# Kernel tuning notes

Hardware: AMD Instinct MI355X
Metric: run time of the kernel (lower is better)

Reference implementation:

```python
import jax, jax.numpy as jnp
import numpy as np

N_LEVELS = 16
N_FEATS = 2
TABLE_SIZE = 1 << 19          # log2_hashmap_size = 19
BASE_RES = 32
PER_LEVEL_SCALE = 1.3819
RES = 512
CLAMP = 25.133
PRIME_Y = np.uint32(2654435761)
N_PTS = 1 << 19


def hashgrid_encode(table, uv):
    """Instant-NGP style multires hashgrid. table: [L, T, F], uv: [N, 2] in [0,1].
    Returns [N, L*F]."""
    L, T, F = table.shape
    levels = jnp.arange(L)
    res = jnp.floor(BASE_RES * (PER_LEVEL_SCALE ** levels.astype(jnp.float32))).astype(jnp.int32)  # [L]
    # 4 bilinear corner offsets
    offs = jnp.array([[0, 0], [1, 0], [0, 1], [1, 1]], dtype=jnp.int32)  # [4, 2]

    def level_fn(tab_l, res_l):
        pos = uv * res_l.astype(uv.dtype)                       # [N, 2]
        p0 = jnp.clip(jnp.floor(pos).astype(jnp.int32), 0, res_l - 1)
        frac = pos - p0.astype(uv.dtype)                        # [N, 2]
        corners = p0[:, None, :] + offs[None, :, :]             # [N, 4, 2]
        cx = corners[..., 0].astype(jnp.uint32)
        cy = corners[..., 1].astype(jnp.uint32)
        stride = (res_l + 1).astype(jnp.uint32)
        dense_idx = cx + cy * stride                            # dense grid index
        hash_idx = (cx ^ (cy * PRIME_Y)) & jnp.uint32(T - 1)    # spatial hash (T is pow2)
        use_dense = (res_l + 1).astype(jnp.int64) * (res_l + 1).astype(jnp.int64) <= T
        idx = jnp.where(use_dense, dense_idx, hash_idx).astype(jnp.int32)  # [N, 4]
        feats = tab_l[idx]                                      # [N, 4, F] gather
        wx, wy = frac[:, 0], frac[:, 1]
        w = jnp.stack([(1 - wx) * (1 - wy), wx * (1 - wy),
                       (1 - wx) * wy, wx * wy], axis=-1)        # [N, 4]
        return jnp.einsum('ncf,nc->nf', feats, w)               # [N, F]

    out = jax.vmap(level_fn)(table, res)                        # [L, N, F]
    return out.transpose(1, 0, 2).reshape(uv.shape[0], L * F)


def sin_layer(x, W, b):
    h = jnp.clip(x @ W.T + b, -CLAMP, CLAMP)
    return jnp.sin(h)


def setup_inputs() -> dict:
    key = jax.random.key(0)
    ks = jax.random.split(key, 8)
    y = jax.random.randint(ks[0], (N_PTS,), 0, RES, dtype=jnp.int32)
    x = jax.random.randint(ks[1], (N_PTS,), 0, RES, dtype=jnp.int32)
    cam_feat = jax.random.normal(ks[2], (32,), dtype=jnp.float32)
    # NGP tables initialized uniform in [-1e-4, 1e-4]
    table = jax.random.uniform(ks[3], (N_LEVELS, TABLE_SIZE, N_FEATS),
                               minval=-1e-4, maxval=1e-4, dtype=jnp.float32)
    def siren_w(k, outp, inp):
        return jax.random.uniform(k, (outp, inp), minval=-1.0 / inp, maxval=1.0 / inp,
                                  dtype=jnp.float32)
    W1 = siren_w(ks[4], 512, 64)
    W2 = siren_w(ks[5], 512, 512)
    W3 = siren_w(ks[6], 384, 512)
    return {"y": y, "x": x, "cam_feat": cam_feat, "table": table,
            "W1": W1, "b1": jnp.zeros((512,), jnp.float32),
            "W2": W2, "b2": jnp.zeros((512,), jnp.float32),
            "W3": W3, "b3": jnp.zeros((384,), jnp.float32)}


def reference(y, x, cam_feat, table, W1, b1, W2, b2, W3, b3):
    denom = jnp.float32(RES - 1)
    uv = jnp.stack([jnp.clip(x.astype(jnp.float32), 0, RES - 1) / denom,
                    jnp.clip(y.astype(jnp.float32), 0, RES - 1) / denom], axis=-1)  # [N, 2]
    codes = hashgrid_encode(table, uv)                          # [N, 32]
    cam = jnp.broadcast_to(cam_feat[None, :], (codes.shape[0], cam_feat.shape[0]))
    h = jnp.concatenate([codes, cam], axis=-1)                  # [N, 64]
    h = sin_layer(h, W1, b1)
    h = sin_layer(h, W2, b2)
    return sin_layer(h, W3, b3)                                 # [N, 384]
```

## Files before the change

### kernel.cpp

```cpp
#include <hip/hip_runtime.h>

typedef _Float16 half8 __attribute__((ext_vector_type(8)));
typedef _Float16 half4 __attribute__((ext_vector_type(4)));
typedef _Float16 half2v __attribute__((ext_vector_type(2)));
typedef float f32x4 __attribute__((ext_vector_type(4)));

#define TSIZE (1 << 19)
#define TMASK (TSIZE - 1)

__constant__ int c_res[16] = {32, 44, 61, 84, 116, 161, 222, 307,
                              425, 588, 812, 1123, 1551, 2144, 2963, 4095};

__global__ void hg_cvt_all(const float* __restrict__ W1, const float* __restrict__ W2,
                           const float* __restrict__ W3, _Float16* __restrict__ d) {
  int g = blockIdx.x * blockDim.x + threadIdx.x;
  int i = g * 4;
  const float* s;
  if (i < 32768) s = W1 + i;
  else if (i < 32768 + 262144) s = W2 + (i - 32768);
  else s = W3 + (i - 32768 - 262144);
  float4 v = *(const float4*)s;
  half4 h = {(_Float16)v.x, (_Float16)v.y, (_Float16)v.z, (_Float16)v.w};
  *(half4*)(d + i) = h;
}

__device__ __forceinline__ float sin_act_precise(float x) {
  if (__builtin_expect(fabsf(x) > 1.0f, 0))
    return sinf(fminf(fmaxf(x, -25.133f), 25.133f));
  float x2 = x * x;
  float p = 2.75573192e-6f;
  p = fmaf(p, x2, -1.98412698e-4f);
  p = fmaf(p, x2, 8.33333333e-3f);
  p = fmaf(p, x2, -1.66666667e-1f);
  return fmaf(p * x2, x, x);
}

__device__ __forceinline__ float sin_act_fast(float x) {
  return __sinf(fminf(fmaxf(x, -25.133f), 25.133f));
}

#define XROW 144
#define SBASE 9216
#define SROW 1040
#define LD_X(m, k) (*(const half8*)(&smem[(m) * XROW + (k) * 2]))
#define LD_S(m, k) (*(const half8*)(&smem[SBASE + (m) * SROW + (k) * 2]))
#define ST_S8(m, n, v) \
  do { *(half4*)(&smem[SBASE + (m) * SROW + (n) * 2]) = (v); } while (0)

#define MFMA16 __builtin_amdgcn_mfma_f32_16x16x32_f16

__global__ void __launch_bounds__(512, 4)
hg_fused(const int* __restrict__ ybuf, const int* __restrict__ xbuf,
         const float* __restrict__ cam, const float* __restrict__ table,
         const _Float16* __restrict__ W1h, const float* __restrict__ b1,
         const _Float16* __restrict__ W2h, const float* __restrict__ b2,
         const _Float16* __restrict__ W3h, const float* __restrict__ b3,
         float* __restrict__ out) {
  __shared__ __align__(16) unsigned char smem[75776];
  const int t = threadIdx.x;
  const int lane = t & 63;
  const int wid = t >> 6;
  const int l15 = lane & 15;
  const int lhi = lane >> 4;
  const int pbase = blockIdx.x << 6;
  const f32x4 vzero = {0.f, 0.f, 0.f, 0.f};

  {
    const int sub = t & 15;
    const int res = c_res[sub];
    const float rf = (float)res;
    const unsigned strd = (unsigned)(res + 1);
    const bool dense = (res <= 723);
    const float* tb = table + ((size_t)sub * TSIZE) * 2;
    const float2 cf = ((const float2*)cam)[sub];
    const half2v hc = {(_Float16)cf.x, (_Float16)cf.y};
#pragma unroll
    for (int hh = 0; hh < 2; ++hh) {
      const int m = (t >> 4) + hh * 32;
      const int p = pbase + m;
      const float u = (float)xbuf[p] / 511.0f;
      const float v = (float)ybuf[p] / 511.0f;
      const float px = u * rf, py = v * rf;
      int p0x = (int)floorf(px); p0x = p0x < 0 ? 0 : (p0x > res - 1 ? res - 1 : p0x);
      int p0y = (int)floorf(py); p0y = p0y < 0 ? 0 : (p0y > res - 1 ? res - 1 : p0y);
      const float fx = px - (float)p0x, fy = py - (float)p0y;
      const float w00 = (1.f - fx) * (1.f - fy), w10 = fx * (1.f - fy);
      const float w01 = (1.f - fx) * fy, w11 = fx * fy;
      float c0 = 0.f, c1 = 0.f;
#pragma unroll
      for (int c = 0; c < 4; ++c) {
        const unsigned cx = (unsigned)(p0x + (c & 1));
        const unsigned cy = (unsigned)(p0y + (c >> 1));
        const unsigned idx = dense ? (cx + cy * strd)
                                   : ((cx ^ (cy * 2654435761u)) & TMASK);
        const float2 f = *(const float2*)(tb + (size_t)idx * 2);
        const float w = (c == 0) ? w00 : (c == 1) ? w10 : (c == 2) ? w01 : w11;
        c0 = fmaf(w, f.x, c0);
        c1 = fmaf(w, f.y, c1);
      }
      half2v hf = {(_Float16)c0, (_Float16)c1};
      *(half2v*)(&smem[m * XROW + 4 * sub]) = hf;
      *(half2v*)(&smem[m * XROW + 64 + 4 * sub]) = hc;
    }
  }
  __syncthreads();

  {
    const int n0 = wid << 6;
    f32x4 acc[4][4];
#pragma unroll
    for (int i = 0; i < 4; ++i)
#pragma unroll
      for (int j = 0; j < 4; ++j) acc[i][j] = vzero;
#pragma unroll
    for (int ks = 0; ks < 2; ++ks) {
      const int kk = ks * 32 + lhi * 8;
      half8 bw[4];
#pragma unroll
      for (int nf = 0; nf < 4; ++nf)
        bw[nf] = *(const half8*)(W1h + (n0 + nf * 16 + l15) * 64 + kk);
      half8 ax[4];
#pragma unroll
      for (int mf = 0; mf < 4; ++mf) ax[mf] = LD_X(mf * 16 + l15, kk);
#pragma unroll
      for (int mf = 0; mf < 4; ++mf)
#pragma unroll
        for (int nf = 0; nf < 4; ++nf)
          acc[mf][nf] = MFMA16(bw[nf], ax[mf], acc[mf][nf], 0, 0, 0);
    }
#pragma unroll
    for (int nf = 0; nf < 4; ++nf) {
      const int nb = n0 + nf * 16 + lhi * 4;
      const f32x4 bb = *(const f32x4*)(b1 + nb);
#pragma unroll
      for (int mf = 0; mf < 4; ++mf) {
        half4 pk;
#pragma unroll
        for (int r = 0; r < 4; ++r)
          pk[r] = (_Float16)sin_act_fast(acc[mf][nf][r] + bb[r]);
        ST_S8(mf * 16 + l15, nb, pk);
      }
    }
  }
  __syncthreads();

  {
    const int n0 = wid << 6;
    f32x4 acc[4][4];
#pragma unroll
    for (int i = 0; i < 4; ++i)
#pragma unroll
      for (int j = 0; j < 4; ++j) acc[i][j] = vzero;
#pragma unroll 2
    for (int ks = 0; ks < 16; ++ks) {
      const int kk = ks * 32 + lhi * 8;
      half8 bw[4];
#pragma unroll
      for (int nf = 0; nf < 4; ++nf)
        bw[nf] = *(const half8*)(W2h + (n0 + nf * 16 + l15) * 512 + kk);
      half8 ax[4];
#pragma unroll
      for (int mf = 0; mf < 4; ++mf) ax[mf] = LD_S(mf * 16 + l15, kk);
#pragma unroll
      for (int mf = 0; mf < 4; ++mf)
#pragma unroll
        for (int nf = 0; nf < 4; ++nf)
          acc[mf][nf] = MFMA16(bw[nf], ax[mf], acc[mf][nf], 0, 0, 0);
    }
#pragma unroll
    for (int nf = 0; nf < 4; ++nf) {
      const f32x4 bb = *(const f32x4*)(b2 + (n0 + nf * 16 + lhi * 4));
#pragma unroll
      for (int mf = 0; mf < 4; ++mf)
#pragma unroll
        for (int r = 0; r < 4; ++r)
          acc[mf][nf][r] = sin_act_fast(acc[mf][nf][r] + bb[r]);
    }
    __syncthreads();
#pragma unroll
    for (int nf = 0; nf < 4; ++nf) {
      const int nb = n0 + nf * 16 + lhi * 4;
#pragma unroll
      for (int mf = 0; mf < 4; ++mf) {
        half4 pk = {(_Float16)acc[mf][nf][0], (_Float16)acc[mf][nf][1],
                    (_Float16)acc[mf][nf][2], (_Float16)acc[mf][nf][3]};
        ST_S8(mf * 16 + l15, nb, pk);
      }
    }
  }
  __syncthreads();

  {
    const int n0 = wid * 48;
    f32x4 acc[4][3];
#pragma unroll
    for (int i = 0; i < 4; ++i)
#pragma unroll
      for (int j = 0; j < 3; ++j) acc[i][j] = vzero;
#pragma unroll 2
    for (int ks = 0; ks < 16; ++ks) {
      const int kk = ks * 32 + lhi * 8;
      half8 bw[3];
#pragma unroll
      for (int nf = 0; nf < 3; ++nf)
        bw[nf] = *(const half8*)(W3h + (n0 + nf * 16 + l15) * 512 + kk);
      half8 ax[4];
#pragma unroll
      for (int mf = 0; mf < 4; ++mf) ax[mf] = LD_S(mf * 16 + l15, kk);
#pragma unroll
      for (int mf = 0; mf < 4; ++mf)
#pragma unroll
        for (int nf = 0; nf < 3; ++nf)
          acc[mf][nf] = MFMA16(bw[nf], ax[mf], acc[mf][nf], 0, 0, 0);
    }
#pragma unroll
    for (int nf = 0; nf < 3; ++nf) {
      const int nb = n0 + nf * 16 + lhi * 4;
      const f32x4 bb = *(const f32x4*)(b3 + nb);
#pragma unroll
      for (int mf = 0; mf < 4; ++mf) {
        float4 o;
        float* op = &o.x;
#pragma unroll
        for (int r = 0; r < 4; ++r)
          op[r] = sin_act_precise(acc[mf][nf][r] + bb[r]);
        *(float4*)(out + (size_t)(pbase + mf * 16 + l15) * 384 + nb) = o;
      }
    }
  }
}

extern "C" void kernel_launch(void* const* d_in, const int* in_sizes, int n_in,
                              void* d_out, int out_size, void* d_ws, size_t ws_size,
                              hipStream_t stream) {
  const int* y = (const int*)d_in[0];
  const int* x = (const int*)d_in[1];
  const float* cam = (const float*)d_in[2];
  const float* table = (const float*)d_in[3];
  const float* W1 = (const float*)d_in[4];
  const float* b1 = (const float*)d_in[5];
  const float* W2 = (const float*)d_in[6];
  const float* b2 = (const float*)d_in[7];
  const float* W3 = (const float*)d_in[8];
  const float* b3 = (const float*)d_in[9];
  float* out = (float*)d_out;

  _Float16* Wh = (_Float16*)d_ws;
  _Float16* W1h = Wh;
  _Float16* W2h = W1h + 512 * 64;
  _Float16* W3h = W2h + 512 * 512;

  hg_cvt_all<<<480, 256, 0, stream>>>(W1, W2, W3, Wh);

  const int nblocks = (1 << 19) / 64;
  hg_fused<<<nblocks, 512, 0, stream>>>(y, x, cam, table, W1h, b1, W2h, b2, W3h, b3, out);
}
```

Measured before the change: 1.145 ms.

## Make fused kernel persistent over 8 tiles with double-buffered activations

Each block now processes eight 64-point tiles instead of one. It issues the hash-grid gather for the next tile during the layer-2 GEMM and computes the next tile's layer 1 into a second shared buffer while layer 3 runs. This is meant to hide gather latency behind MFMA work and to amortize the block prologue. In exchange it doubles shared memory to about 139 KB, which drops occupancy to fewer blocks per CU, and leaves only 1024 blocks for the whole GPU. The clamp is also switched to a single fmed3 instruction.

```diff
diff --git a/kernel.cpp b/kernel.cpp
--- a/kernel.cpp
+++ b/kernel.cpp
@@ -7,6 +7,7 @@
 
 #define TSIZE (1 << 19)
 #define TMASK (TSIZE - 1)
+#define NT 8
 
 __constant__ int c_res[16] = {32, 44, 61, 84, 116, 161, 222, 307,
                               425, 588, 812, 1123, 1551, 2144, 2963, 4095};
@@ -36,36 +37,37 @@
 }
 
 __device__ __forceinline__ float sin_act_fast(float x) {
-  return __sinf(fminf(fmaxf(x, -25.133f), 25.133f));
+  return __sinf(__builtin_amdgcn_fmed3f(x, -25.133f, 25.133f));
 }
 
 #define XROW 144
-#define SBASE 9216
 #define SROW 1040
+#define SB0 9216
+#define SB1 75776
 #define LD_X(m, k) (*(const half8*)(&smem[(m) * XROW + (k) * 2]))
-#define LD_S(m, k) (*(const half8*)(&smem[SBASE + (m) * SROW + (k) * 2]))
-#define ST_S8(m, n, v) \
-  do { *(half4*)(&smem[SBASE + (m) * SROW + (n) * 2]) = (v); } while (0)
+#define LD_S(base, m, k) (*(const half8*)(&smem[(base) + (m) * SROW + (k) * 2]))
+#define ST_S8(base, m, n, v) \
+  do { *(half4*)(&smem[(base) + (m) * SROW + (n) * 2]) = (v); } while (0)
 
 #define MFMA16 __builtin_amdgcn_mfma_f32_16x16x32_f16
 
-__global__ void __launch_bounds__(512, 4)
+__global__ void __launch_bounds__(512, 2)
 hg_fused(const int* __restrict__ ybuf, const int* __restrict__ xbuf,
          const float* __restrict__ cam, const float* __restrict__ table,
          const _Float16* __restrict__ W1h, const float* __restrict__ b1,
          const _Float16* __restrict__ W2h, const float* __restrict__ b2,
          const _Float16* __restrict__ W3h, const float* __restrict__ b3,
          float* __restrict__ out) {
-  __shared__ __align__(16) unsigned char smem[75776];
+  __shared__ __align__(16) unsigned char smem[142336];
   const int t = threadIdx.x;
   const int lane = t & 63;
   const int wid = t >> 6;
   const int l15 = lane & 15;
   const int lhi = lane >> 4;
-  const int pbase = blockIdx.x << 6;
+  const int blk0 = blockIdx.x << 9;
   const f32x4 vzero = {0.f, 0.f, 0.f, 0.f};
 
-  {
+  auto ENC = [&](int tile) {
     const int sub = t & 15;
     const int res = c_res[sub];
     const float rf = (float)res;
@@ -74,10 +76,11 @@
     const float* tb = table + ((size_t)sub * TSIZE) * 2;
     const float2 cf = ((const float2*)cam)[sub];
     const half2v hc = {(_Float16)cf.x, (_Float16)cf.y};
+    const int pb = blk0 + (tile << 6);
 #pragma unroll
     for (int hh = 0; hh < 2; ++hh) {
       const int m = (t >> 4) + hh * 32;
-      const int p = pbase + m;
+      const int p = pb + m;
       const float u = (float)xbuf[p] / 511.0f;
       const float v = (float)ybuf[p] / 511.0f;
       const float px = u * rf, py = v * rf;
@@ -102,10 +105,9 @@
       *(half2v*)(&smem[m * XROW + 4 * sub]) = hf;
       *(half2v*)(&smem[m * XROW + 64 + 4 * sub]) = hc;
     }
-  }
-  __syncthreads();
-
-  {
+  };
+
+  auto L1F = [&](int sb) {
     const int n0 = wid << 6;
     f32x4 acc[4][4];
 #pragma unroll
@@ -138,19 +140,27 @@
 #pragma unroll
         for (int r = 0; r < 4; ++r)
           pk[r] = (_Float16)sin_act_fast(acc[mf][nf][r] + bb[r]);
-        ST_S8(mf * 16 + l15, nb, pk);
-      }
-    }
-  }
+        ST_S8(sb, mf * 16 + l15, nb, pk);
+      }
+    }
+  };
+
+  ENC(0);
   __syncthreads();
-
-  {
+  L1F(SB0);
+  __syncthreads();
+
+  for (int tt = 0; tt < NT; ++tt) {
+    const int sb = (tt & 1) ? SB1 : SB0;
+    const int sbn = (tt & 1) ? SB0 : SB1;
     const int n0 = wid << 6;
-    f32x4 acc[4][4];
+
+    f32x4 acc2[4][4];
 #pragma unroll
     for (int i = 0; i < 4; ++i)
 #pragma unroll
-      for (int j = 0; j < 4; ++j) acc[i][j] = vzero;
+      for (int j = 0; j < 4; ++j) acc2[i][j] = vzero;
+    if (tt + 1 < NT) ENC(tt + 1);
 #pragma unroll 2
     for (int ks = 0; ks < 16; ++ks) {
       const int kk = ks * 32 + lhi * 8;
@@ -160,12 +170,12 @@
         bw[nf] = *(const half8*)(W2h + (n0 + nf * 16 + l15) * 512 + kk);
       half8 ax[4];
 #pragma unroll
-      for (int mf = 0; mf < 4; ++mf) ax[mf] = LD_S(mf * 16 + l15, kk);
+      for (int mf = 0; mf < 4; ++mf) ax[mf] = LD_S(sb, mf * 16 + l15, kk);
 #pragma unroll
       for (int mf = 0; mf < 4; ++mf)
 #pragma unroll
         for (int nf = 0; nf < 4; ++nf)
-          acc[mf][nf] = MFMA16(bw[nf], ax[mf], acc[mf][nf], 0, 0, 0);
+          acc2[mf][nf] = MFMA16(bw[nf], ax[mf], acc2[mf][nf], 0, 0, 0);
     }
 #pragma unroll
     for (int nf = 0; nf < 4; ++nf) {
@@ -174,59 +184,63 @@
       for (int mf = 0; mf < 4; ++mf)
 #pragma unroll
         for (int r = 0; r < 4; ++r)
-          acc[mf][nf][r] = sin_act_fast(acc[mf][nf][r] + bb[r]);
+          acc2[mf][nf][r] = sin_act_fast(acc2[mf][nf][r] + bb[r]);
     }
     __syncthreads();
+
 #pragma unroll
     for (int nf = 0; nf < 4; ++nf) {
       const int nb = n0 + nf * 16 + lhi * 4;
 #pragma unroll
       for (int mf = 0; mf < 4; ++mf) {
-        half4 pk = {(_Float16)acc[mf][nf][0], (_Float16)acc[mf][nf][1],
-                    (_Float16)acc[mf][nf][2], (_Float16)acc[mf][nf][3]};
-        ST_S8(mf * 16 + l15, nb, pk);
-      }
-    }
-  }
-  __syncthreads();
-
-  {
-    const int n0 = wid * 48;
-    f32x4 acc[4][3];
-#pragma unroll
-    for (int i = 0; i < 4; ++i)
-#pragma unroll
-      for (int j = 0; j < 3; ++j) acc[i][j] = vzero;
+        half4 pk = {(_Float16)acc2[mf][nf][0], (_Float16)acc2[mf][nf][1],
+                    (_Float16)acc2[mf][nf][2], (_Float16)acc2[mf][nf][3]};
+        ST_S8(sb, mf * 16 + l15, nb, pk);
+      }
+    }
+    __syncthreads();
+
+    if (tt + 1 < NT) L1F(sbn);
+    {
+      const int c0n = wid * 48;
+      f32x4 acc3[4][3];
+#pragma unroll
+      for (int i = 0; i < 4; ++i)
+#pragma unroll
+        for (int j = 0; j < 3; ++j) acc3[i][j] = vzero;
 #pragma unroll 2
-    for (int ks = 0; ks < 16; ++ks) {
-      const int kk = ks * 32 + lhi * 8;
-      half8 bw[3];
-#pragma unroll
-      for (int nf = 0; nf < 3; ++nf)
-        bw[nf] = *(const half8*)(W3h + (n0 + nf * 16 + l15) * 512 + kk);
-      half8 ax[4];
-#pragma unroll
-      for (int mf = 0; mf < 4; ++mf) ax[mf] = LD_S(mf * 16 + l15, kk);
-#pragma unroll
-      for (int mf = 0; mf < 4; ++mf)
+      for (int ks = 0; ks < 16; ++ks) {
+        const int kk = ks * 32 + lhi * 8;
+        half8 bw[3];
 #pragma unroll
         for (int nf = 0; nf < 3; ++nf)
-          acc[mf][nf] = MFMA16(bw[nf], ax[mf], acc[mf][nf], 0, 0, 0);
-    }
-#pragma unroll
-    for (int nf = 0; nf < 3; ++nf) {
-      const int nb = n0 + nf * 16 + lhi * 4;
-      const f32x4 bb = *(const f32x4*)(b3 + nb);
-#pragma unroll
-      for (int mf = 0; mf < 4; ++mf) {
-        float4 o;
-        float* op = &o.x;
-#pragma unroll
-        for (int r = 0; r < 4; ++r)
-          op[r] = sin_act_precise(acc[mf][nf][r] + bb[r]);
-        *(float4*)(out + (size_t)(pbase + mf * 16 + l15) * 384 + nb) = o;
-      }
-    }
+          bw[nf] = *(const half8*)(W3h + (c0n + nf * 16 + l15) * 512 + kk);
+        half8 ax[4];
+#pragma unroll
+        for (int mf = 0; mf < 4; ++mf) ax[mf] = LD_S(sb, mf * 16 + l15, kk);
+#pragma unroll
+        for (int mf = 0; mf < 4; ++mf)
+#pragma unroll
+          for (int nf = 0; nf < 3; ++nf)
+            acc3[mf][nf] = MFMA16(bw[nf], ax[mf], acc3[mf][nf], 0, 0, 0);
+      }
+      const int pb = blk0 + (tt << 6);
+#pragma unroll
+      for (int nf = 0; nf < 3; ++nf) {
+        const int nb = c0n + nf * 16 + lhi * 4;
+        const f32x4 bb = *(const f32x4*)(b3 + nb);
+#pragma unroll
+        for (int mf = 0; mf < 4; ++mf) {
+          float4 o;
+          float* op = &o.x;
+#pragma unroll
+          for (int r = 0; r < 4; ++r)
+            op[r] = sin_act_precise(acc3[mf][nf][r] + bb[r]);
+          *(float4*)(out + (size_t)(pb + mf * 16 + l15) * 384 + nb) = o;
+        }
+      }
+    }
+    __syncthreads();
   }
 }
 
@@ -252,6 +266,6 @@
 
   hg_cvt_all<<<480, 256, 0, stream>>>(W1, W2, W3, Wh);
 
-  const int nblocks = (1 << 19) / 64;
+  const int nblocks = (1 << 19) / 512;
   hg_fused<<<nblocks, 512, 0, stream>>>(y, x, cam, table, W1h, b1, W2h, b2, W3h, b3, out);
 }
```

Measured after the change: 1.301 ms. 1.14x slower.
